# Optimization experiments

Hardware: AMD Instinct MI355X
Metric: run time of the kernel (lower is better)

Reference implementation:

```python
import jax, jax.numpy as jnp
import numpy as np

B, T, C = 4, 2048, 1024
H, D = 16, 64          # n_head, head_dim; H*D == C
FFN = 4096
EPS = 1e-6


def rmsnorm(x, w):
    rms = jnp.sqrt(jnp.mean(x * x, axis=-1, keepdims=True) + EPS)
    return x / rms * w


def l2norm(x):
    n = jnp.sqrt(jnp.sum(x * x, axis=-1, keepdims=True))
    return x / jnp.maximum(n, 1e-12)


def setup_inputs() -> dict:
    key = jax.random.key(0)
    ks = jax.random.split(key, 16)
    s = 0.02
    inp = {
        'x': jax.random.normal(ks[0], (B, T, C), jnp.float32),
        'cos': jax.random.uniform(ks[1], (T, D // 2), jnp.float32),
        'sin': jax.random.uniform(ks[2], (T, D // 2), jnp.float32),
        'norm1_w': jnp.ones((C,), jnp.float32),
        'norm2_w': jnp.ones((C,), jnp.float32),
        'q_w': jax.random.normal(ks[3], (C, C), jnp.float32) * s,
        'k_w': jax.random.normal(ks[4], (C, C), jnp.float32) * s,
        'v_w': jax.random.normal(ks[5], (C, C), jnp.float32) * s,
        'beta_w': jax.random.normal(ks[6], (H, C), jnp.float32) * s,
        'beta_b': jnp.zeros((H,), jnp.float32),
        'gate_w': jax.random.normal(ks[7], (C, C), jnp.float32) * s,
        'o_w': jax.random.normal(ks[8], (C, C), jnp.float32) * s,
        'ffn_gate_w': jax.random.normal(ks[9], (FFN, C), jnp.float32) * s,
        'ffn_up_w': jax.random.normal(ks[10], (FFN, C), jnp.float32) * s,
        'ffn_down_w': jax.random.normal(ks[11], (C, FFN), jnp.float32) * s,
    }
    return inp


def gated_delta_net(xn, q_w, k_w, v_w, beta_w, beta_b, gate_w, o_w):
    # projections -> (B, T, H, D)
    q = (xn @ q_w.T).reshape(B, T, H, D)
    k = (xn @ k_w.T).reshape(B, T, H, D)
    v = (xn @ v_w.T).reshape(B, T, H, D)
    beta = jax.nn.sigmoid(xn @ beta_w.T + beta_b)   # (B, T, H)
    gate = jax.nn.sigmoid(xn @ gate_w.T)            # (B, T, C)
    q = l2norm(q)
    k = l2norm(k)

    # time-major for scan: (T, B, H, D)
    qs = jnp.moveaxis(q, 1, 0)
    ks = jnp.moveaxis(k, 1, 0)
    vs = jnp.moveaxis(v, 1, 0)
    bs = jnp.moveaxis(beta, 1, 0)                   # (T, B, H)

    def step(M, inp):
        q_t, k_t, v_t, b_t = inp
        o_t = jnp.einsum('bhdc,bhc->bhd', M, q_t)
        dv = v_t - jnp.einsum('bhdc,bhc->bhd', M, k_t)
        M = M + b_t[:, :, None, None] * jnp.einsum('bhd,bhc->bhdc', dv, k_t)
        return M, o_t

    M0 = jnp.zeros((B, H, D, D), xn.dtype)
    _, os = jax.lax.scan(step, M0, (qs, ks, vs, bs))  # os: (T, B, H, D)
    o = jnp.moveaxis(os, 0, 1).reshape(B, T, C)
    return (gate * o) @ o_w.T


def swiglu(xn, gate_w, up_w, down_w):
    return (jax.nn.silu(xn @ gate_w.T) * (xn @ up_w.T)) @ down_w.T


def reference(x, cos, sin, norm1_w, norm2_w, q_w, k_w, v_w, beta_w, beta_b,
              gate_w, o_w, ffn_gate_w, ffn_up_w, ffn_down_w):
    # layer_idx=0 -> GatedDeltaNet branch (cos/sin unused, as in torch module)
    x = x + gated_delta_net(rmsnorm(x, norm1_w), q_w, k_w, v_w,
                            beta_w, beta_b, gate_w, o_w)
    x = x + swiglu(rmsnorm(x, norm2_w), ffn_gate_w, ffn_up_w, ffn_down_w)
    return x
```

## Files before the change

### kernel.cpp

```cpp
#include <hip/hip_runtime.h>
#include <stdint.h>

typedef unsigned short u16;
typedef unsigned int   u32;
typedef unsigned long long u64;

typedef __bf16 bf16x8 __attribute__((ext_vector_type(8)));
typedef u16    u16x8  __attribute__((ext_vector_type(8)));
typedef u16    u16x4  __attribute__((ext_vector_type(4)));
typedef float  f32x4  __attribute__((ext_vector_type(4)));

#define BQ 4
#define TT 2048
#define CC 1024
#define HH 16
#define DD 64
#define FF 4096
#define BT 8192
#define NCH 32
#define LCH 64
#define LS 72

__device__ __forceinline__ float b2f(u16 v) {
  u32 u = ((u32)v) << 16;
  return __builtin_bit_cast(float, u);
}
__device__ __forceinline__ u16 f2b(float f) {
  u32 u = __builtin_bit_cast(u32, f);
  u32 r = (u + 0x7fffu + ((u >> 16) & 1u)) >> 16;
  return (u16)r;
}
__device__ __forceinline__ bf16x8 ld8(const u16* p) {
  return __builtin_bit_cast(bf16x8, *(const u16x8*)p);
}
__device__ __forceinline__ float sigmoidf_(float x) {
  return 1.0f / (1.0f + __expf(-x));
}

#define MFMA16(a, b, c) __builtin_amdgcn_mfma_f32_16x16x32_bf16(a, b, c, 0, 0, 0)

__device__ __forceinline__ void stage16(const u16* g, u16* lds_base) {
  __builtin_amdgcn_global_load_lds(
      (const __attribute__((address_space(1))) u32*)(uintptr_t)g,
      (__attribute__((address_space(3))) u32*)lds_base, 16, 0, 0);
}

struct Cvt { const float* src; u16* dst; u32 n; u32 pad; };
struct CvtArgs { Cvt d[12]; };

__global__ __launch_bounds__(256) void convert_k(CvtArgs a)
{
  const Cvt c = a.d[blockIdx.y];
  u64 i = ((u64)blockIdx.x * 256 + threadIdx.x) * 8;
  if (i >= c.n) return;
  f32x4 v0 = *(const f32x4*)(c.src + i);
  f32x4 v1 = *(const f32x4*)(c.src + i + 4);
  u16x8 o;
#pragma unroll
  for (int e = 0; e < 4; ++e) { o[e] = f2b(v0[e]); o[e + 4] = f2b(v1[e]); }
  *(u16x8*)(c.dst + i) = o;
}

template <int MODE>
__global__ __launch_bounds__(256) void gemm_bt(
    const u16* __restrict__ A, const u16* __restrict__ Bw,
    void* __restrict__ Cv, const void* __restrict__ res,
    int M, int N, int K)
{
  __shared__ __align__(16) u16 As[128 * 32];
  __shared__ __align__(16) u16 Bs[128 * 32];
  const int tid  = threadIdx.x;
  const int lane = tid & 63;
  const int wave = tid >> 6;
  const int bm = blockIdx.x, bn = blockIdx.y;
  const int rw = lane >> 2;
  const int kq = (lane & 3) * 8;
  const int lo = lane & 15;
  const int quad = lane >> 4;
  const int wm = wave & 1, wn = wave >> 1;

  const u16* Ag = A  + (u64)(bm * 128 + wave * 16 + rw) * K + kq;
  const u16* Bg = Bw + (u64)(bn * 128 + wave * 16 + rw) * K + kq;
  u16* As0 = As + wave * 16 * 32;
  u16* Bs0 = Bs + wave * 16 * 32;

  f32x4 acc[4][4] = {};

  for (int k0 = 0; k0 < K; k0 += 32) {
    stage16(Ag + k0, As0);
    stage16(Ag + (u64)64 * K + k0, As0 + 64 * 32);
    stage16(Bg + k0, Bs0);
    stage16(Bg + (u64)64 * K + k0, Bs0 + 64 * 32);
    __syncthreads();
    bf16x8 af[4], bq[4];
#pragma unroll
    for (int i = 0; i < 4; ++i)
      af[i] = ld8(As + (wm * 64 + i * 16 + lo) * 32 + quad * 8);
#pragma unroll
    for (int j = 0; j < 4; ++j)
      bq[j] = ld8(Bs + (wn * 64 + j * 16 + lo) * 32 + quad * 8);
#pragma unroll
    for (int i = 0; i < 4; ++i)
#pragma unroll
      for (int j = 0; j < 4; ++j)
        acc[i][j] = MFMA16(af[i], bq[j], acc[i][j]);
    __syncthreads();
  }

  u16* C16 = (u16*)Cv;
  float* C32 = (float*)Cv;
  const float* R32 = (const float*)res;
  const u16* R16 = (const u16*)res;
#pragma unroll
  for (int i = 0; i < 4; ++i)
#pragma unroll
    for (int j = 0; j < 4; ++j)
#pragma unroll
      for (int r = 0; r < 4; ++r) {
        int row = bm * 128 + wm * 64 + i * 16 + quad * 4 + r;
        int col = bn * 128 + wn * 64 + j * 16 + lo;
        u64 off = (u64)row * N + col;
        float v = acc[i][j][r];
        if (MODE == 1) { v += R32[off]; C16[off] = f2b(v); }
        else if (MODE == 2) { v += b2f(R16[off]); C32[off] = v; }
        else if (MODE == 3) {
          float g = b2f(R16[off]);
          C16[off] = f2b(g * sigmoidf_(g) * v);
        } else C16[off] = f2b(v);
      }
}

template <int IN32>
__global__ __launch_bounds__(256) void rmsnorm_k(
    const void* __restrict__ xv, const u16* __restrict__ w, u16* __restrict__ out)
{
  __shared__ float red[4];
  const int row = blockIdx.x, tid = threadIdx.x;
  float v0, v1, v2, v3;
  if (IN32) {
    f32x4 raw = *(const f32x4*)((const float*)xv + (u64)row * CC + tid * 4);
    v0 = raw[0]; v1 = raw[1]; v2 = raw[2]; v3 = raw[3];
  } else {
    u16x4 raw = *(const u16x4*)((const u16*)xv + (u64)row * CC + tid * 4);
    v0 = b2f(raw[0]); v1 = b2f(raw[1]); v2 = b2f(raw[2]); v3 = b2f(raw[3]);
  }
  float s = v0 * v0 + v1 * v1 + v2 * v2 + v3 * v3;
#pragma unroll
  for (int m = 1; m < 64; m <<= 1) s += __shfl_xor(s, m, 64);
  if ((tid & 63) == 0) red[tid >> 6] = s;
  __syncthreads();
  float tot = red[0] + red[1] + red[2] + red[3];
  float r = rsqrtf(tot * (1.0f / CC) + 1e-6f);
  const u16* wr = w + tid * 4;
  u16x4 o;
  o[0] = f2b(v0 * r * b2f(wr[0]));
  o[1] = f2b(v1 * r * b2f(wr[1]));
  o[2] = f2b(v2 * r * b2f(wr[2]));
  o[3] = f2b(v3 * r * b2f(wr[3]));
  *(u16x4*)(out + (u64)row * CC + tid * 4) = o;
}

__global__ __launch_bounds__(256) void l2norm_k(u16* __restrict__ q)
{
  const int row = blockIdx.x, tid = threadIdx.x;
  const int hh = tid >> 4, ss = tid & 15;
  u16* p = q + (u64)row * CC + hh * DD + ss * 4;
  u16x4 raw = *(const u16x4*)p;
  float v0 = b2f(raw[0]), v1 = b2f(raw[1]), v2 = b2f(raw[2]), v3 = b2f(raw[3]);
  float s = v0 * v0 + v1 * v1 + v2 * v2 + v3 * v3;
#pragma unroll
  for (int m = 1; m < 16; m <<= 1) s += __shfl_xor(s, m, 64);
  float sc = 1.0f / fmaxf(sqrtf(s), 1e-12f);
  u16x4 o;
  o[0] = f2b(v0 * sc); o[1] = f2b(v1 * sc);
  o[2] = f2b(v2 * sc); o[3] = f2b(v3 * sc);
  *(u16x4*)p = o;
}

__global__ __launch_bounds__(256) void beta_k(
    const u16* __restrict__ xn, const u16* __restrict__ bw,
    const u16* __restrict__ bb, float* __restrict__ beta)
{
  const int row = blockIdx.x, tid = threadIdx.x;
  const int hh = tid >> 4, ss = tid & 15;
  const u16* xr = xn + (u64)row * CC + ss * 64;
  const u16* wr = bw + (u64)hh * CC + ss * 64;
  float s = 0.f;
#pragma unroll
  for (int j = 0; j < 8; ++j) {
    u16x8 a = *(const u16x8*)(xr + j * 8);
    u16x8 c = *(const u16x8*)(wr + j * 8);
#pragma unroll
    for (int e = 0; e < 8; ++e) s += b2f(a[e]) * b2f(c[e]);
  }
#pragma unroll
  for (int m = 1; m < 16; m <<= 1) s += __shfl_xor(s, m, 64);
  if (ss == 0) beta[(u64)row * HH + hh] = sigmoidf_(s + b2f(bb[hh]));
}

__global__ __launch_bounds__(256) void chunk_pre(
    const u16* __restrict__ qn, const u16* __restrict__ kn,
    const u16* __restrict__ vn, const float* __restrict__ beta,
    u16* __restrict__ wneg, u16* __restrict__ u0m, u16* __restrict__ pm)
{
  __shared__ __align__(16) u16 Qc[64 * LS], Kc[64 * LS], Vc[64 * LS];
  __shared__ float Af[64 * 64];
  __shared__ float bet[64];
  const int tid = threadIdx.x;
  const int lane = tid & 63, wave = tid >> 6;
  const int lo = lane & 15, quad = lane >> 4;
  const int bc = blockIdx.x;
  const int bh = bc >> 5, c = bc & 31;
  const int b = bh >> 4, h = bh & 15;
  const u64 gbase = ((u64)(b * TT + c * LCH) * HH + h) * DD;
  const u64 cb = (u64)bc * 4096;

#pragma unroll
  for (int it = 0; it < 2; ++it) {
    int idx = tid + it * 256;
    int t = idx >> 3, seg = (idx & 7) * 8;
    u64 g = gbase + (u64)t * CC + seg;
    *(u16x8*)(Qc + t * LS + seg) = *(const u16x8*)(qn + g);
    *(u16x8*)(Kc + t * LS + seg) = *(const u16x8*)(kn + g);
    *(u16x8*)(Vc + t * LS + seg) = *(const u16x8*)(vn + g);
  }
  if (tid < 64) bet[tid] = beta[(u64)(b * TT + c * LCH + tid) * HH + h];
  __syncthreads();

  {
    const int wm = wave & 1, wn = wave >> 1;
    f32x4 aa[2][2] = {};
#pragma unroll
    for (int k0 = 0; k0 < 64; k0 += 32) {
      bf16x8 af[2], bq[2];
#pragma unroll
      for (int i = 0; i < 2; ++i) af[i] = ld8(Kc + (wm * 32 + i * 16 + lo) * LS + k0 + quad * 8);
#pragma unroll
      for (int j = 0; j < 2; ++j) bq[j] = ld8(Kc + (wn * 32 + j * 16 + lo) * LS + k0 + quad * 8);
#pragma unroll
      for (int i = 0; i < 2; ++i)
#pragma unroll
        for (int j = 0; j < 2; ++j) aa[i][j] = MFMA16(af[i], bq[j], aa[i][j]);
    }
#pragma unroll
    for (int i = 0; i < 2; ++i)
#pragma unroll
      for (int j = 0; j < 2; ++j)
#pragma unroll
        for (int r = 0; r < 4; ++r) {
          int t = wm * 32 + i * 16 + quad * 4 + r;
          int s = wn * 32 + j * 16 + lo;
          Af[t * 64 + s] = (s < t) ? bet[t] * aa[i][j][r] : 0.0f;
        }
  }
  __syncthreads();

  if (wave < 2) {
    const u16* src = (wave == 0) ? Kc : Vc;
    u16* dst = (wave == 0) ? wneg : u0m;
    const float sgn = (wave == 0) ? -1.0f : 1.0f;
    const int d = lane;
    float hist[64];
#pragma unroll
    for (int t = 0; t < 64; ++t) {
      float a = bet[t] * b2f(src[t * LS + d]);
#pragma unroll
      for (int s = 0; s < t; ++s) a -= Af[t * 64 + s] * hist[s];
      hist[t] = a;
      dst[cb + (u64)t * 64 + d] = f2b(sgn * a);
    }
  } else {
    const int w2 = wave - 2;
    f32x4 ap[2][4] = {};
#pragma unroll
    for (int k0 = 0; k0 < 64; k0 += 32) {
      bf16x8 af[2], bq[4];
#pragma unroll
      for (int i = 0; i < 2; ++i) af[i] = ld8(Qc + (w2 * 32 + i * 16 + lo) * LS + k0 + quad * 8);
#pragma unroll
      for (int j = 0; j < 4; ++j) bq[j] = ld8(Kc + (j * 16 + lo) * LS + k0 + quad * 8);
#pragma unroll
      for (int i = 0; i < 2; ++i)
#pragma unroll
        for (int j = 0; j < 4; ++j) ap[i][j] = MFMA16(af[i], bq[j], ap[i][j]);
    }
#pragma unroll
    for (int i = 0; i < 2; ++i)
#pragma unroll
      for (int j = 0; j < 4; ++j)
#pragma unroll
        for (int r = 0; r < 4; ++r) {
          int t = w2 * 32 + i * 16 + quad * 4 + r;
          int s = j * 16 + lo;
          pm[cb + (u64)t * 64 + s] = f2b((s < t) ? ap[i][j][r] : 0.0f);
        }
  }
}

__global__ __launch_bounds__(256) void chunk_seq(
    const u16* __restrict__ qn, const u16* __restrict__ kn,
    const u16* __restrict__ wneg, const u16* __restrict__ u0m,
    const u16* __restrict__ pm, u16* __restrict__ ob)
{
  __shared__ __align__(16) u16 Qs[64 * LS], KTs[64 * LS], Ws[64 * LS], Ps[64 * LS];
  __shared__ __align__(16) u16 U0q[64 * 16];
  __shared__ __align__(16) u16 Sq[16 * LS], UTq[16 * LS];
  const int tid = threadIdx.x;
  const int lane = tid & 63, wave = tid >> 6;
  const int lo = lane & 15, quad = lane >> 4;
  const int blk = blockIdx.x;
  const int bh = blk >> 2, q = blk & 3;
  const int b = bh >> 4, h = bh & 15;
  f32x4 Sacc = {};

  for (int i = tid; i < 16 * LS; i += 256) Sq[i] = 0;
  __syncthreads();

#pragma unroll 1
  for (int c = 0; c < NCH; ++c) {
    const u64 gbase = ((u64)(b * TT + c * LCH) * HH + h) * DD;
    const u64 cb = (u64)(bh * NCH + c) * 4096;
#pragma unroll
    for (int it = 0; it < 2; ++it) {
      int idx = tid + it * 256;
      int t = idx >> 3, seg = (idx & 7) * 8;
      u64 g = gbase + (u64)t * CC + seg;
      *(u16x8*)(Qs + t * LS + seg) = *(const u16x8*)(qn + g);
      u16x8 kv = *(const u16x8*)(kn + g);
#pragma unroll
      for (int jj = 0; jj < 8; ++jj) KTs[(seg + jj) * LS + t] = kv[jj];
      *(u16x8*)(Ws + t * LS + seg) = *(const u16x8*)(wneg + cb + t * 64 + seg);
      *(u16x8*)(Ps + t * LS + seg) = *(const u16x8*)(pm + cb + t * 64 + seg);
    }
    if (tid < 128) {
      int t = tid >> 1, half = (tid & 1) * 8;
      *(u16x8*)(U0q + t * 16 + half) =
          *(const u16x8*)(u0m + cb + t * 64 + q * 16 + half);
    }
    __syncthreads();

    f32x4 au;
#pragma unroll
    for (int r = 0; r < 4; ++r)
      au[r] = b2f(U0q[(wave * 16 + quad * 4 + r) * 16 + lo]);
#pragma unroll
    for (int k0 = 0; k0 < 64; k0 += 32) {
      bf16x8 af = ld8(Ws + (wave * 16 + lo) * LS + k0 + quad * 8);
      bf16x8 bq = ld8(Sq + lo * LS + k0 + quad * 8);
      au = MFMA16(af, bq, au);
    }
#pragma unroll
    for (int r = 0; r < 4; ++r)
      UTq[lo * LS + wave * 16 + quad * 4 + r] = f2b(au[r]);
    __syncthreads();

    f32x4 ao = {};
#pragma unroll
    for (int k0 = 0; k0 < 64; k0 += 32) {
      bf16x8 af = ld8(Qs + (wave * 16 + lo) * LS + k0 + quad * 8);
      bf16x8 bq = ld8(Sq + lo * LS + k0 + quad * 8);
      ao = MFMA16(af, bq, ao);
    }
#pragma unroll
    for (int k0 = 0; k0 < 64; k0 += 32) {
      bf16x8 af = ld8(Ps + (wave * 16 + lo) * LS + k0 + quad * 8);
      bf16x8 bq = ld8(UTq + lo * LS + k0 + quad * 8);
      ao = MFMA16(af, bq, ao);
    }
#pragma unroll
    for (int r = 0; r < 4; ++r)
      ob[gbase + (u64)(wave * 16 + quad * 4 + r) * CC + q * 16 + lo] = f2b(ao[r]);

#pragma unroll
    for (int k0 = 0; k0 < 64; k0 += 32) {
      bf16x8 af = ld8(UTq + lo * LS + k0 + quad * 8);
      bf16x8 bq = ld8(KTs + (wave * 16 + lo) * LS + k0 + quad * 8);
      Sacc = MFMA16(af, bq, Sacc);
    }
    __syncthreads();
#pragma unroll
    for (int r = 0; r < 4; ++r)
      Sq[(quad * 4 + r) * LS + wave * 16 + lo] = f2b(Sacc[r]);
    __syncthreads();
  }
}

__global__ __launch_bounds__(256) void gate_mul_k(const u16* __restrict__ g,
                                                  u16* __restrict__ o, u64 n)
{
  u64 i = ((u64)blockIdx.x * 256 + threadIdx.x) * 8;
  if (i >= n) return;
  u16x8 gv = *(const u16x8*)(g + i);
  u16x8 ov = *(const u16x8*)(o + i);
  u16x8 r;
#pragma unroll
  for (int e = 0; e < 8; ++e)
    r[e] = f2b(sigmoidf_(b2f(gv[e])) * b2f(ov[e]));
  *(u16x8*)(o + i) = r;
}

extern "C" void kernel_launch(void* const* d_in, const int* in_sizes, int n_in,
                              void* d_out, int out_size, void* d_ws, size_t ws_size,
                              hipStream_t stream)
{
  (void)in_sizes; (void)n_in; (void)out_size; (void)ws_size;
  const float* x32 = (const float*)d_in[0];
  char* ws = (char*)d_ws;
  const u64 SZ = (u64)BT * CC * 2;
  const u64 MB = 1ull << 20;

  u16* xn1  = (u16*)(ws + 0 * SZ);
  u16* qb   = (u16*)(ws + 1 * SZ);
  u16* kb   = (u16*)(ws + 2 * SZ);
  u16* vb   = (u16*)(ws + 3 * SZ);
  u16* grw  = (u16*)(ws + 4 * SZ);
  u16* wneg = (u16*)(ws + 5 * SZ);
  u16* u0m  = (u16*)(ws + 6 * SZ);
  u16* pmm  = (u16*)(ws + 7 * SZ);
  u16* obf  = (u16*)(ws + 8 * SZ);
  u16* x2   = (u16*)(ws + 9 * SZ);
  float* beta = (float*)(ws + 10 * SZ);
  char* CV  = ws + 10 * SZ + MB;
  u16* qwc  = (u16*)(CV + 0 * MB);
  u16* kwc  = (u16*)(CV + 2 * MB);
  u16* vwc  = (u16*)(CV + 4 * MB);
  u16* gwc  = (u16*)(CV + 6 * MB);
  u16* owc  = (u16*)(CV + 8 * MB);
  u16* fgwc = (u16*)(CV + 10 * MB);
  u16* fuwc = (u16*)(CV + 18 * MB);
  u16* fdwc = (u16*)(CV + 26 * MB);
  u16* bwc  = (u16*)(CV + 34 * MB);
  u16* n1c  = (u16*)(CV + 34 * MB + 64 * 1024);
  u16* n2c  = (u16*)(CV + 34 * MB + 80 * 1024);
  u16* bbc  = (u16*)(CV + 34 * MB + 96 * 1024);
  u16* ffg  = (u16*)(ws + 0 * SZ);
  u16* ffu  = (u16*)(ws + 4 * SZ);
  u16* xn2  = obf;

  dim3 blk(256);
  dim3 g1(BT / 128, CC / 128);
  dim3 g2(BT / 128, FF / 128);
  u64 ne = (u64)BT * CC;

  CvtArgs ca;
  ca.d[0]  = { (const float*)d_in[5],  qwc,  (u32)(CC * CC), 0 };
  ca.d[1]  = { (const float*)d_in[6],  kwc,  (u32)(CC * CC), 0 };
  ca.d[2]  = { (const float*)d_in[7],  vwc,  (u32)(CC * CC), 0 };
  ca.d[3]  = { (const float*)d_in[10], gwc,  (u32)(CC * CC), 0 };
  ca.d[4]  = { (const float*)d_in[11], owc,  (u32)(CC * CC), 0 };
  ca.d[5]  = { (const float*)d_in[12], fgwc, (u32)(FF * CC), 0 };
  ca.d[6]  = { (const float*)d_in[13], fuwc, (u32)(FF * CC), 0 };
  ca.d[7]  = { (const float*)d_in[14], fdwc, (u32)(CC * FF), 0 };
  ca.d[8]  = { (const float*)d_in[8],  bwc,  (u32)(HH * CC), 0 };
  ca.d[9]  = { (const float*)d_in[3],  n1c,  (u32)CC, 0 };
  ca.d[10] = { (const float*)d_in[4],  n2c,  (u32)CC, 0 };
  ca.d[11] = { (const float*)d_in[9],  bbc,  (u32)HH, 0 };
  convert_k<<<dim3(2048, 12), blk, 0, stream>>>(ca);

  rmsnorm_k<1><<<BT, blk, 0, stream>>>(x32, n1c, xn1);
  gemm_bt<0><<<g1, blk, 0, stream>>>(xn1, qwc, qb, nullptr, BT, CC, CC);
  gemm_bt<0><<<g1, blk, 0, stream>>>(xn1, kwc, kb, nullptr, BT, CC, CC);
  gemm_bt<0><<<g1, blk, 0, stream>>>(xn1, vwc, vb, nullptr, BT, CC, CC);
  gemm_bt<0><<<g1, blk, 0, stream>>>(xn1, gwc, grw, nullptr, BT, CC, CC);
  beta_k<<<BT, blk, 0, stream>>>(xn1, bwc, bbc, beta);
  l2norm_k<<<BT, blk, 0, stream>>>(qb);
  l2norm_k<<<BT, blk, 0, stream>>>(kb);
  chunk_pre<<<BQ * HH * NCH, blk, 0, stream>>>(qb, kb, vb, beta, wneg, u0m, pmm);
  chunk_seq<<<BQ * HH * 4, blk, 0, stream>>>(qb, kb, wneg, u0m, pmm, obf);
  gate_mul_k<<<(unsigned)(ne / 8 / 256), blk, 0, stream>>>(grw, obf, ne);
  gemm_bt<1><<<g1, blk, 0, stream>>>(obf, owc, x2, x32, BT, CC, CC);
  rmsnorm_k<0><<<BT, blk, 0, stream>>>(x2, n2c, xn2);
  gemm_bt<0><<<g2, blk, 0, stream>>>(xn2, fgwc, ffg, nullptr, BT, FF, CC);
  gemm_bt<3><<<g2, blk, 0, stream>>>(xn2, fuwc, ffg, ffg, BT, FF, CC);
  gemm_bt<2><<<g1, blk, 0, stream>>>(ffg, fdwc, d_out, x2, BT, CC, FF);
}
```

Baseline: 830.6 us.

## Double-buffer GEMM LDS tiles, vectorize epilogue via LDS, fuse gating into chunk_seq

The GEMM now double-buffers its A/B LDS tiles, prefetching the next K-slice while the current one is consumed, which removes one barrier per iteration. The epilogue for the bf16 modes stages results through padded LDS so global stores and residual/gate loads are 16-byte coalesced vectors instead of scattered scalar accesses. The separate sigmoid-gate multiply kernel is folded into chunk_seq's output write, saving one elementwise pass over the activation. LDS use per block grows, which may reduce occupancy, and the epilogue rounds the accumulator to bf16 before adding the residual, which adds a small precision change.

```diff
diff --git a/kernel.cpp b/kernel.cpp
--- a/kernel.cpp
+++ b/kernel.cpp
@@ -20,6 +20,7 @@
 #define NCH 32
 #define LCH 64
 #define LS 72
+#define SE 140
 
 __device__ __forceinline__ float b2f(u16 v) {
   u32 u = ((u32)v) << 16;
@@ -67,8 +68,7 @@
     void* __restrict__ Cv, const void* __restrict__ res,
     int M, int N, int K)
 {
-  __shared__ __align__(16) u16 As[128 * 32];
-  __shared__ __align__(16) u16 Bs[128 * 32];
+  __shared__ __align__(16) u16 smem[128 * SE];
   const int tid  = threadIdx.x;
   const int lane = tid & 63;
   const int wave = tid >> 6;
@@ -81,53 +81,104 @@
 
   const u16* Ag = A  + (u64)(bm * 128 + wave * 16 + rw) * K + kq;
   const u16* Bg = Bw + (u64)(bn * 128 + wave * 16 + rw) * K + kq;
-  u16* As0 = As + wave * 16 * 32;
-  u16* Bs0 = Bs + wave * 16 * 32;
+  u16* const Ab[2] = { smem + wave * 512, smem + 4096 + wave * 512 };
+  u16* const Bb[2] = { smem + 8192 + wave * 512, smem + 12288 + wave * 512 };
 
   f32x4 acc[4][4] = {};
-
-  for (int k0 = 0; k0 < K; k0 += 32) {
-    stage16(Ag + k0, As0);
-    stage16(Ag + (u64)64 * K + k0, As0 + 64 * 32);
-    stage16(Bg + k0, Bs0);
-    stage16(Bg + (u64)64 * K + k0, Bs0 + 64 * 32);
+  const int niter = K >> 5;
+
+  stage16(Ag, Ab[0]);
+  stage16(Ag + (u64)64 * K, Ab[0] + 2048);
+  stage16(Bg, Bb[0]);
+  stage16(Bg + (u64)64 * K, Bb[0] + 2048);
+
+  int cur = 0;
+  for (int it = 0; it < niter; ++it) {
     __syncthreads();
+    if (it + 1 < niter) {
+      int kn = (it + 1) << 5;
+      stage16(Ag + kn, Ab[cur ^ 1]);
+      stage16(Ag + (u64)64 * K + kn, Ab[cur ^ 1] + 2048);
+      stage16(Bg + kn, Bb[cur ^ 1]);
+      stage16(Bg + (u64)64 * K + kn, Bb[cur ^ 1] + 2048);
+    }
+    const u16* Ac = smem + cur * 4096;
+    const u16* Bc = smem + 8192 + cur * 4096;
     bf16x8 af[4], bq[4];
 #pragma unroll
     for (int i = 0; i < 4; ++i)
-      af[i] = ld8(As + (wm * 64 + i * 16 + lo) * 32 + quad * 8);
+      af[i] = ld8(Ac + (wm * 64 + i * 16 + lo) * 32 + quad * 8);
 #pragma unroll
     for (int j = 0; j < 4; ++j)
-      bq[j] = ld8(Bs + (wn * 64 + j * 16 + lo) * 32 + quad * 8);
+      bq[j] = ld8(Bc + (wn * 64 + j * 16 + lo) * 32 + quad * 8);
 #pragma unroll
     for (int i = 0; i < 4; ++i)
 #pragma unroll
       for (int j = 0; j < 4; ++j)
         acc[i][j] = MFMA16(af[i], bq[j], acc[i][j]);
-    __syncthreads();
-  }
+    cur ^= 1;
+  }
+
+  if (MODE == 2) {
+    const u16* R16 = (const u16*)res;
+    float* C32 = (float*)Cv;
+#pragma unroll
+    for (int i = 0; i < 4; ++i)
+#pragma unroll
+      for (int j = 0; j < 4; ++j)
+#pragma unroll
+        for (int r = 0; r < 4; ++r) {
+          int row = bm * 128 + wm * 64 + i * 16 + quad * 4 + r;
+          int col = bn * 128 + wn * 64 + j * 16 + lo;
+          u64 off = (u64)row * N + col;
+          C32[off] = acc[i][j][r] + b2f(R16[off]);
+        }
+    return;
+  }
+
+  __syncthreads();
+#pragma unroll
+  for (int i = 0; i < 4; ++i)
+#pragma unroll
+    for (int j = 0; j < 4; ++j)
+#pragma unroll
+      for (int r = 0; r < 4; ++r)
+        smem[(wm * 64 + i * 16 + quad * 4 + r) * SE + wn * 64 + j * 16 + lo] =
+            f2b(acc[i][j][r]);
+  __syncthreads();
 
   u16* C16 = (u16*)Cv;
-  float* C32 = (float*)Cv;
   const float* R32 = (const float*)res;
   const u16* R16 = (const u16*)res;
-#pragma unroll
-  for (int i = 0; i < 4; ++i)
-#pragma unroll
-    for (int j = 0; j < 4; ++j)
-#pragma unroll
-      for (int r = 0; r < 4; ++r) {
-        int row = bm * 128 + wm * 64 + i * 16 + quad * 4 + r;
-        int col = bn * 128 + wn * 64 + j * 16 + lo;
-        u64 off = (u64)row * N + col;
-        float v = acc[i][j][r];
-        if (MODE == 1) { v += R32[off]; C16[off] = f2b(v); }
-        else if (MODE == 2) { v += b2f(R16[off]); C32[off] = v; }
-        else if (MODE == 3) {
-          float g = b2f(R16[off]);
-          C16[off] = f2b(g * sigmoidf_(g) * v);
-        } else C16[off] = f2b(v);
+  const int orow = tid >> 4, ocol = (tid & 15) * 8;
+#pragma unroll
+  for (int w = 0; w < 8; ++w) {
+    int rl = orow + w * 16;
+    u16x8 v = *(const u16x8*)(smem + rl * SE + ocol);
+    u64 off = (u64)(bm * 128 + rl) * N + bn * 128 + ocol;
+    if (MODE == 0) {
+      *(u16x8*)(C16 + off) = v;
+    } else if (MODE == 1) {
+      f32x4 r0 = *(const f32x4*)(R32 + off);
+      f32x4 r1 = *(const f32x4*)(R32 + off + 4);
+      u16x8 o;
+#pragma unroll
+      for (int e = 0; e < 4; ++e) {
+        o[e]     = f2b(b2f(v[e])     + r0[e]);
+        o[e + 4] = f2b(b2f(v[e + 4]) + r1[e]);
       }
+      *(u16x8*)(C16 + off) = o;
+    } else {
+      u16x8 g = *(const u16x8*)(R16 + off);
+      u16x8 o;
+#pragma unroll
+      for (int e = 0; e < 8; ++e) {
+        float gg = b2f(g[e]);
+        o[e] = f2b(gg * sigmoidf_(gg) * b2f(v[e]));
+      }
+      *(u16x8*)(C16 + off) = o;
+    }
+  }
 }
 
 template <int IN32>
@@ -300,7 +351,8 @@
 __global__ __launch_bounds__(256) void chunk_seq(
     const u16* __restrict__ qn, const u16* __restrict__ kn,
     const u16* __restrict__ wneg, const u16* __restrict__ u0m,
-    const u16* __restrict__ pm, u16* __restrict__ ob)
+    const u16* __restrict__ pm, const u16* __restrict__ gate,
+    u16* __restrict__ ob)
 {
   __shared__ __align__(16) u16 Qs[64 * LS], KTs[64 * LS], Ws[64 * LS], Ps[64 * LS];
   __shared__ __align__(16) u16 U0q[64 * 16];
@@ -368,8 +420,11 @@
       ao = MFMA16(af, bq, ao);
     }
 #pragma unroll
-    for (int r = 0; r < 4; ++r)
-      ob[gbase + (u64)(wave * 16 + quad * 4 + r) * CC + q * 16 + lo] = f2b(ao[r]);
+    for (int r = 0; r < 4; ++r) {
+      u64 gidx = gbase + (u64)(wave * 16 + quad * 4 + r) * CC + q * 16 + lo;
+      float gg = b2f(gate[gidx]);
+      ob[gidx] = f2b(sigmoidf_(gg) * ao[r]);
+    }
 
 #pragma unroll
     for (int k0 = 0; k0 < 64; k0 += 32) {
@@ -383,20 +438,6 @@
       Sq[(quad * 4 + r) * LS + wave * 16 + lo] = f2b(Sacc[r]);
     __syncthreads();
   }
-}
-
-__global__ __launch_bounds__(256) void gate_mul_k(const u16* __restrict__ g,
-                                                  u16* __restrict__ o, u64 n)
-{
-  u64 i = ((u64)blockIdx.x * 256 + threadIdx.x) * 8;
-  if (i >= n) return;
-  u16x8 gv = *(const u16x8*)(g + i);
-  u16x8 ov = *(const u16x8*)(o + i);
-  u16x8 r;
-#pragma unroll
-  for (int e = 0; e < 8; ++e)
-    r[e] = f2b(sigmoidf_(b2f(gv[e])) * b2f(ov[e]));
-  *(u16x8*)(o + i) = r;
 }
 
 extern "C" void kernel_launch(void* const* d_in, const int* in_sizes, int n_in,
@@ -434,13 +475,11 @@
   u16* n2c  = (u16*)(CV + 34 * MB + 80 * 1024);
   u16* bbc  = (u16*)(CV + 34 * MB + 96 * 1024);
   u16* ffg  = (u16*)(ws + 0 * SZ);
-  u16* ffu  = (u16*)(ws + 4 * SZ);
   u16* xn2  = obf;
 
   dim3 blk(256);
   dim3 g1(BT / 128, CC / 128);
   dim3 g2(BT / 128, FF / 128);
-  u64 ne = (u64)BT * CC;
 
   CvtArgs ca;
   ca.d[0]  = { (const float*)d_in[5],  qwc,  (u32)(CC * CC), 0 };
@@ -466,8 +505,7 @@
   l2norm_k<<<BT, blk, 0, stream>>>(qb);
   l2norm_k<<<BT, blk, 0, stream>>>(kb);
   chunk_pre<<<BQ * HH * NCH, blk, 0, stream>>>(qb, kb, vb, beta, wneg, u0m, pmm);
-  chunk_seq<<<BQ * HH * 4, blk, 0, stream>>>(qb, kb, wneg, u0m, pmm, obf);
-  gate_mul_k<<<(unsigned)(ne / 8 / 256), blk, 0, stream>>>(grw, obf, ne);
+  chunk_seq<<<BQ * HH * 4, blk, 0, stream>>>(qb, kb, wneg, u0m, pmm, grw, obf);
   gemm_bt<1><<<g1, blk, 0, stream>>>(obf, owc, x2, x32, BT, CC, CC);
   rmsnorm_k<0><<<BT, blk, 0, stream>>>(x2, n2c, xn2);
   gemm_bt<0><<<g2, blk, 0, stream>>>(xn2, fgwc, ffg, nullptr, BT, FF, CC);
```

Measured after the change: 767.0 us. 1.08x faster.
